# Optimization experiments

Measured on AMD Instinct MI355X. Metric: run time of the kernel, lower is better.

Reference implementation:

```python
import jax, jax.numpy as jnp
import numpy as np
import math

H = 300
B = 2048
SEG = 48
N = B * SEG

def _gru_direction(x_seq, h0, w_ih, w_hh, b_ih, b_hh, reverse):
    # x_seq: [L, B, H]; h0: [B, H]; w_ih/w_hh: [3H, H]; b_ih/b_hh: [3H]
    xp = jnp.einsum('lbh,gh->lbg', x_seq, w_ih) + b_ih  # precompute input projections [L,B,3H]
    def step(h, xp_t):
        hp = h @ w_hh.T + b_hh
        xr, xz, xn = jnp.split(xp_t, 3, axis=-1)
        hr, hz, hn = jnp.split(hp, 3, axis=-1)
        r = jax.nn.sigmoid(xr + hr)
        z = jax.nn.sigmoid(xz + hz)
        n = jnp.tanh(xn + r * hn)
        h_new = (1.0 - z) * n + z * h
        return h_new, h_new
    _, ys = jax.lax.scan(step, h0, xp, reverse=reverse)
    return ys  # [L, B, H]

def setup_inputs() -> dict:
    key = jax.random.key(0)
    ks = jax.random.split(key, 12)
    bound = 1.0 / math.sqrt(H)
    u = lambda k, shape: jax.random.uniform(k, shape, jnp.float32, -bound, bound)
    x = jax.random.normal(ks[0], (N, H), jnp.float32)
    batch = jnp.repeat(jnp.arange(B, dtype=jnp.int32), SEG)  # sorted segment ids
    return {
        'x': x,
        'batch': batch,
        'num_moles': B,
        'max_len': SEG,
        'bias': u(ks[1], (H,)),
        'w_ih_f': u(ks[2], (3 * H, H)),
        'w_hh_f': u(ks[3], (3 * H, H)),
        'b_ih_f': u(ks[4], (3 * H,)),
        'b_hh_f': u(ks[5], (3 * H,)),
        'w_ih_b': u(ks[6], (3 * H, H)),
        'w_hh_b': u(ks[7], (3 * H, H)),
        'b_ih_b': u(ks[8], (3 * H,)),
        'b_hh_b': u(ks[9], (3 * H,)),
    }

def reference(x, batch, num_moles, max_len, bias, w_ih_f, w_hh_f, b_ih_f, b_hh_f, w_ih_b, w_hh_b, b_ih_b, b_hh_b):
    n, h = x.shape
    message = jax.nn.relu(x + bias)
    counts = jax.ops.segment_sum(jnp.ones_like(batch), batch, num_segments=num_moles)
    offsets = jnp.cumsum(counts) - counts
    pos = jnp.arange(n, dtype=batch.dtype) - offsets[batch]  # position within molecule
    # ragged -> padded pack [B, L, H]
    padded = jnp.zeros((num_moles, max_len, h), x.dtype).at[batch, pos].set(message)
    # initial hidden = per-molecule max over raw x (same h0 for both directions)
    h0 = jax.ops.segment_max(x, batch, num_segments=num_moles)  # [B, H]
    xs = padded.transpose(1, 0, 2)  # [L, B, H]
    yf = _gru_direction(xs, h0, w_ih_f, w_hh_f, b_ih_f, b_hh_f, reverse=False)
    yb = _gru_direction(xs, h0, w_ih_b, w_hh_b, b_ih_b, b_hh_b, reverse=True)
    y = jnp.concatenate([yf, yb], axis=-1).transpose(1, 0, 2)  # [B, L, 2H]
    return y[batch, pos]  # unpad -> [N, 2H]
```

## Files before the change

### kernel.cpp

```cpp
#include <hip/hip_runtime.h>
#include <hip/hip_bf16.h>

#define H    300
#define KP   320
#define BM   2048
#define SEG  48
#define NTOK (BM*SEG)
#define G    900
#define GW   1024
#define XPW  912
#define MOLW 16
#define NCH  10
#define BKX  64

typedef __attribute__((ext_vector_type(8))) short short8;
typedef __attribute__((ext_vector_type(4))) float f32x4;

__device__ __forceinline__ float us2f(unsigned short u) { return __uint_as_float(((unsigned)u) << 16); }
__device__ __forceinline__ unsigned short bfb(float f) {
    __hip_bfloat16 b = __float2bfloat16(f);
    return *(unsigned short*)&b;
}
__device__ __forceinline__ void gload16(const void* g, void* l) {
    __builtin_amdgcn_global_load_lds((const __attribute__((address_space(1))) unsigned*)g,
                                     (__attribute__((address_space(3))) unsigned*)l, 16, 0, 0);
}

__global__ void prep_weights(const float* wih_f, const float* whh_f, const float* bih_f,
                             const float* wih_b, const float* whh_b, const float* bih_b,
                             __hip_bfloat16* wih, __hip_bfloat16* whh, float* bih) {
    int idx = blockIdx.x * 256 + threadIdx.x;
    const int wn = 2 * GW * KP;
    if (idx < wn) {
        int d = idx / (GW * KP);
        int R = (idx / KP) % GW;
        int k = idx % KP;
        int ct = R / 48, rem = R % 48, g = rem / 16, i = rem % 16;
        int col = ct * 16 + i;
        const float* src = d ? wih_b : wih_f;
        float v = (R < 912 && col < H && k < H) ? src[(g * H + col) * H + k] : 0.f;
        wih[idx] = __float2bfloat16(v);
        return;
    }
    idx -= wn;
    if (idx < wn) {
        int d = idx / (GW * KP);
        int R = (idx / KP) % GW;
        int k = idx % KP;
        int ct = R / 48, rem = R % 48, g = rem / 16, i = rem % 16;
        int col = ct * 16 + i;
        const float* src = d ? whh_b : whh_f;
        float v = (R < 912 && col < H && k < H) ? src[(g * H + col) * H + k] : 0.f;
        whh[idx] = __float2bfloat16(v);
        return;
    }
    idx -= wn;
    if (idx < 2 * GW) {
        int d = idx / GW;
        int R = idx % GW;
        int ct = R / 48, rem = R % 48, g = rem / 16, i = rem % 16;
        int col = ct * 16 + i;
        const float* src = d ? bih_b : bih_f;
        bih[idx] = (R < 912 && col < H) ? src[g * H + col] : 0.f;
    }
}

__global__ void prep_msg(const float* x, const float* bias, __hip_bfloat16* msg) {
    int idx = blockIdx.x * 256 + threadIdx.x;
    if (idx >= NTOK * KP) return;
    int i = idx / KP, k = idx % KP;
    float v = 0.f;
    if (k < H) {
        v = x[i * H + k] + bias[k];
        v = v > 0.f ? v : 0.f;
    }
    msg[idx] = __float2bfloat16(v);
}

__global__ void h0_kernel(const float* x, float* h0) {
    int m = blockIdx.x;
    for (int c = threadIdx.x; c < H; c += blockDim.x) {
        const float* base = x + (long long)m * SEG * H + c;
        float v = -INFINITY;
        for (int t = 0; t < SEG; t++) v = fmaxf(v, base[t * H]);
        h0[m * H + c] = v;
    }
}

__global__ __launch_bounds__(256) void xp_gemm(const __hip_bfloat16* msg, const __hip_bfloat16* wih,
                                               const float* bih, __hip_bfloat16* xp) {
    int d = blockIdx.z;
    const __hip_bfloat16* A  = msg;
    const __hip_bfloat16* Bw = wih + d * GW * KP;
    const float* bi = bih + d * GW;
    __hip_bfloat16* out = xp + (long long)d * NTOK * XPW;

    __shared__ __hip_bfloat16 sA[128 * BKX];
    __shared__ __hip_bfloat16 sB[128 * BKX];
    const short* sAs = (const short*)sA;
    const short* sBs = (const short*)sB;

    int tid = threadIdx.x;
    int lane = tid & 63, wid = tid >> 6;
    int l15 = lane & 15, quad = lane >> 4;
    int mblk = blockIdx.x * 128, nblk = blockIdx.y * 128;
    int mbase = (wid >> 1) * 64, nbase = (wid & 1) * 64;

    int srow = wid * 32 + (lane >> 3);
    int scc  = (lane & 7) ^ (srow & 7);
    const short* gA0 = (const short*)A  + (long long)(mblk + srow) * KP + scc * 8;
    const short* gB0 = (const short*)Bw + (long long)(nblk + srow) * KP + scc * 8;
    int xsw = (l15 & 7) << 3;

    f32x4 acc[4][4] = {};
    for (int kc = 0; kc < KP / BKX; kc++) {
#pragma unroll
        for (int j = 0; j < 4; j++)
            gload16(gA0 + (long long)j * 8 * KP + kc * BKX, (char*)sA + (wid * 4 + j) * 1024);
#pragma unroll
        for (int j = 0; j < 4; j++)
            gload16(gB0 + (long long)j * 8 * KP + kc * BKX, (char*)sB + (wid * 4 + j) * 1024);
        __syncthreads();

        short8 af[4][2], bf[4][2];
#pragma unroll
        for (int i = 0; i < 4; i++)
#pragma unroll
            for (int kh = 0; kh < 2; kh++)
                af[i][kh] = *(const short8*)(sAs + (mbase + i * 16 + l15) * BKX + ((kh * 32 + quad * 8) ^ xsw));
#pragma unroll
        for (int j = 0; j < 4; j++)
#pragma unroll
            for (int kh = 0; kh < 2; kh++)
                bf[j][kh] = *(const short8*)(sBs + (nbase + j * 16 + l15) * BKX + ((kh * 32 + quad * 8) ^ xsw));
#pragma unroll
        for (int i = 0; i < 4; i++)
#pragma unroll
            for (int j = 0; j < 4; j++) {
                acc[i][j] = __builtin_amdgcn_mfma_f32_16x16x32_bf16(af[i][0], bf[j][0], acc[i][j], 0, 0, 0);
                acc[i][j] = __builtin_amdgcn_mfma_f32_16x16x32_bf16(af[i][1], bf[j][1], acc[i][j], 0, 0, 0);
            }
        __syncthreads();
    }

#pragma unroll
    for (int i = 0; i < 4; i++)
#pragma unroll
        for (int j = 0; j < 4; j++) {
            int col = nblk + nbase + j * 16 + l15;
            if (col < XPW) {
                float bv = bi[col];
#pragma unroll
                for (int r = 0; r < 4; r++) {
                    int row = mblk + mbase + i * 16 + quad * 4 + r;
                    out[(long long)row * XPW + col] = __float2bfloat16(acc[i][j][r] + bv);
                }
            }
        }
}

__global__ __launch_bounds__(1024) void gru_kernel(const __hip_bfloat16* whh_all, const float* bhh_f,
                                                   const float* bhh_b, const __hip_bfloat16* xp,
                                                   const float* h0, float* out) {
    int grp = blockIdx.x;
    int d   = blockIdx.y;
    const char* whhd = (const char*)(whh_all + (long long)d * GW * KP);
    const float* bhh = d ? bhh_b : bhh_f;
    const __hip_bfloat16* xpd = xp + (long long)d * NTOK * XPW;

    int tid = threadIdx.x;
    int lane = tid & 63, wid = tid >> 6;
    int l15 = lane & 15, quad = lane >> 4;
    int xor3 = (l15 & 3) ^ ((l15 >> 2) & 3);

    __shared__ __hip_bfloat16 hB[MOLW * 328];
    __shared__ char bufA[65536];
    __shared__ char bufB[65536];

    int mol0 = grp * MOLW;

    const char* dmasrc[4];
#pragma unroll
    for (int j = 0; j < 4; j++) {
        int R = (wid * 4 + j) * 16 + (lane >> 2);
        int s = lane & 3;
        int sw = s ^ (R & 3) ^ ((R >> 2) & 3);
        dmasrc[j] = whhd + R * (KP * 2) + sw * 16;
    }

    int nct = (wid < 3) ? 2 : 1;

    for (int e = tid; e < MOLW * 328; e += 1024) hB[e] = __float2bfloat16(0.f);
    __syncthreads();

    float bvv[2][3];
    f32x4 hreg[2];
#pragma unroll
    for (int cc = 0; cc < 2; cc++) {
        if (cc < nct) {
            int ct = cc ? 16 + wid : wid;
            int col = ct * 16 + l15;
            bool cv = col < H;
#pragma unroll
            for (int g = 0; g < 3; g++)
                bvv[cc][g] = cv ? bhh[g * H + col] : 0.f;
#pragma unroll
            for (int r = 0; r < 4; r++) {
                float hv = cv ? h0[(size_t)(mol0 + quad * 4 + r) * H + col] : 0.f;
                hreg[cc][r] = hv;
                if (cv) hB[(quad * 4 + r) * 328 + col] = __float2bfloat16(hv);
            }
        }
    }

#pragma unroll
    for (int j = 0; j < 4; j++)
        gload16(dmasrc[j], bufA + (wid * 4 + j) * 1024);
    __syncthreads();

    for (int t = 0; t < SEG; t++) {
        int tt = d ? (SEG - 1 - t) : t;

        f32x4 acc[2][3] = {};
        unsigned short xv[2][3][4];

        auto phase = [&](int c, const char* curb, char* nxtb) {
            int nk = (c + 1) % NCH;
#pragma unroll
            for (int j = 0; j < 4; j++)
                gload16(dmasrc[j] + nk * 64, nxtb + (wid * 4 + j) * 1024);
            if (c == 8) {
#pragma unroll
                for (int cc = 0; cc < 2; cc++)
                    if (cc < nct) {
                        int ct = cc ? 16 + wid : wid;
#pragma unroll
                        for (int r = 0; r < 4; r++) {
                            long long tok = (long long)(mol0 + quad * 4 + r) * SEG + tt;
                            const unsigned short* xrow = (const unsigned short*)(xpd + tok * XPW + ct * 48 + l15);
#pragma unroll
                            for (int g = 0; g < 3; g++)
                                xv[cc][g][r] = xrow[g * 16];
                        }
                    }
            }
            short8 aq = *(const short8*)((const char*)hB + l15 * 656 + c * 64 + quad * 16);
#pragma unroll
            for (int cc = 0; cc < 2; cc++)
                if (cc < nct) {
                    int ct = cc ? 16 + wid : wid;
#pragma unroll
                    for (int g = 0; g < 3; g++) {
                        short8 bq = *(const short8*)(curb + (ct * 48 + g * 16 + l15) * 64 + ((quad ^ xor3) << 4));
                        acc[cc][g] = __builtin_amdgcn_mfma_f32_16x16x32_bf16(aq, bq, acc[cc][g], 0, 0, 0);
                    }
                }
            __syncthreads();
        };

#pragma unroll
        for (int c2 = 0; c2 < 5; c2++) {
            phase(2 * c2,     bufA, bufB);
            phase(2 * c2 + 1, bufB, bufA);
        }

#pragma unroll
        for (int cc = 0; cc < 2; cc++)
            if (cc < nct) {
                int ct = cc ? 16 + wid : wid;
                int col = ct * 16 + l15;
                bool cv = col < H;
#pragma unroll
                for (int r = 0; r < 4; r++) {
                    float hr = acc[cc][0][r] + bvv[cc][0];
                    float hz = acc[cc][1][r] + bvv[cc][1];
                    float hn = acc[cc][2][r] + bvv[cc][2];
                    float xr = us2f(xv[cc][0][r]);
                    float xz = us2f(xv[cc][1][r]);
                    float xn = us2f(xv[cc][2][r]);
                    float rg = 1.f / (1.f + __expf(-(xr + hr)));
                    float zg = 1.f / (1.f + __expf(-(xz + hz)));
                    float ni = xn + rg * hn;
                    float ng = 1.f - 2.f / (__expf(2.f * ni) + 1.f);
                    float hnew = (1.f - zg) * ng + zg * hreg[cc][r];
                    hreg[cc][r] = hnew;
                    if (cv) {
                        hB[(quad * 4 + r) * 328 + col] = __float2bfloat16(hnew);
                        long long tok = (long long)(mol0 + quad * 4 + r) * SEG + tt;
                        out[tok * 600 + d * 300 + col] = hnew;
                    }
                }
            }
        __syncthreads();
    }
}

extern "C" void kernel_launch(void* const* d_in, const int* in_sizes, int n_in,
                              void* d_out, int out_size, void* d_ws, size_t ws_size,
                              hipStream_t stream) {
    const float* x     = (const float*)d_in[0];
    const float* bias  = (const float*)d_in[4];
    const float* wih_f = (const float*)d_in[5];
    const float* whh_f = (const float*)d_in[6];
    const float* bih_f = (const float*)d_in[7];
    const float* bhh_f = (const float*)d_in[8];
    const float* wih_b = (const float*)d_in[9];
    const float* whh_b = (const float*)d_in[10];
    const float* bih_b = (const float*)d_in[11];
    const float* bhh_b = (const float*)d_in[12];
    float* out = (float*)d_out;

    char* ws = (char*)d_ws;
    __hip_bfloat16* msg = (__hip_bfloat16*)(ws);
    __hip_bfloat16* wih = (__hip_bfloat16*)(ws + 62914560LL);
    __hip_bfloat16* whh = (__hip_bfloat16*)(ws + 64225280LL);
    float*          bih = (float*)         (ws + 65536000LL);
    float*          h0  = (float*)         (ws + 65544192LL);
    __hip_bfloat16* xp  = (__hip_bfloat16*)(ws + 68001792LL);

    hipLaunchKernelGGL(prep_weights, dim3((2*GW*KP + 2*GW*KP + 2*GW + 255) / 256), dim3(256), 0, stream,
                       wih_f, whh_f, bih_f, wih_b, whh_b, bih_b, wih, whh, bih);
    hipLaunchKernelGGL(prep_msg, dim3((NTOK * KP + 255) / 256), dim3(256), 0, stream, x, bias, msg);
    hipLaunchKernelGGL(h0_kernel, dim3(BM), dim3(256), 0, stream, x, h0);
    hipLaunchKernelGGL(xp_gemm, dim3(NTOK / 128, GW / 128, 2), dim3(256), 0, stream, msg, wih, bih, xp);
    hipLaunchKernelGGL(gru_kernel, dim3(BM / MOLW, 2), dim3(1024), 0, stream, whh, bhh_f, bhh_b, xp, h0, out);
}
```

Before: 1.810 ms.

## Restructure GRU recurrence kernel: 32 molecules per block, staged gate epilogue

Each GRU block now processes 32 molecules instead of 16 using 512 threads. Every streamed W_hh chunk now feeds two MFMAs (two 16-row A tiles), which halves the weight traffic per molecule. The hidden projection is written as bf16 into the spent LDS buffer, and a separate element-pair pass computes the gates with vectorized xp/out accesses. It also uses explicit waitcnt/barrier pipelining and a block-index remap for the 128 blocks. In exchange, hp is rounded to bf16, each step gains an extra LDS round trip and barriers, and there are half as many blocks.

```diff
diff --git a/kernel.cpp b/kernel.cpp
--- a/kernel.cpp
+++ b/kernel.cpp
@@ -9,14 +9,18 @@
 #define G    900
 #define GW   1024
 #define XPW  912
-#define MOLW 16
+#define MOLW 32
+#define NPAIR (MOLW*150)
+#define PIT  10
+#define NT   57
 #define NCH  10
 #define BKX  64
 
 typedef __attribute__((ext_vector_type(8))) short short8;
 typedef __attribute__((ext_vector_type(4))) float f32x4;
 
-__device__ __forceinline__ float us2f(unsigned short u) { return __uint_as_float(((unsigned)u) << 16); }
+__device__ __forceinline__ float lo16(unsigned u) { return __uint_as_float(u << 16); }
+__device__ __forceinline__ float hi16(unsigned u) { return __uint_as_float(u & 0xffff0000u); }
 __device__ __forceinline__ unsigned short bfb(float f) {
     __hip_bfloat16 b = __float2bfloat16(f);
     return *(unsigned short*)&b;
@@ -25,6 +29,7 @@
     __builtin_amdgcn_global_load_lds((const __attribute__((address_space(1))) unsigned*)g,
                                      (__attribute__((address_space(3))) unsigned*)l, 16, 0, 0);
 }
+#define LBAR() do { asm volatile("s_waitcnt lgkmcnt(0)" ::: "memory"); __builtin_amdgcn_s_barrier(); } while (0)
 
 __global__ void prep_weights(const float* wih_f, const float* whh_f, const float* bih_f,
                              const float* wih_b, const float* whh_b, const float* bih_b,
@@ -159,11 +164,12 @@
         }
 }
 
-__global__ __launch_bounds__(1024) void gru_kernel(const __hip_bfloat16* whh_all, const float* bhh_f,
-                                                   const float* bhh_b, const __hip_bfloat16* xp,
-                                                   const float* h0, float* out) {
-    int grp = blockIdx.x;
-    int d   = blockIdx.y;
+__global__ __launch_bounds__(512, 2) void gru_kernel(const __hip_bfloat16* whh_all, const float* bhh_f,
+                                                     const float* bhh_b, const __hip_bfloat16* xp,
+                                                     const float* h0, float* out) {
+    int b = blockIdx.x;
+    int d = (b >> 2) & 1;
+    int grp = (b >> 3) * 4 + (b & 3);
     const char* whhd = (const char*)(whh_all + (long long)d * GW * KP);
     const float* bhh = d ? bhh_b : bhh_f;
     const __hip_bfloat16* xpd = xp + (long long)d * NTOK * XPW;
@@ -171,7 +177,6 @@
     int tid = threadIdx.x;
     int lane = tid & 63, wid = tid >> 6;
     int l15 = lane & 15, quad = lane >> 4;
-    int xor3 = (l15 & 3) ^ ((l15 >> 2) & 3);
 
     __shared__ __hip_bfloat16 hB[MOLW * 328];
     __shared__ char bufA[65536];
@@ -179,119 +184,150 @@
 
     int mol0 = grp * MOLW;
 
-    const char* dmasrc[4];
-#pragma unroll
-    for (int j = 0; j < 4; j++) {
-        int R = (wid * 4 + j) * 16 + (lane >> 2);
-        int s = lane & 3;
-        int sw = s ^ (R & 3) ^ ((R >> 2) & 3);
-        dmasrc[j] = whhd + R * (KP * 2) + sw * 16;
-    }
-
-    int nct = (wid < 3) ? 2 : 1;
-
-    for (int e = tid; e < MOLW * 328; e += 1024) hB[e] = __float2bfloat16(0.f);
+    const char* sb[8];
+#pragma unroll
+    for (int j = 0; j < 8; j++) {
+        int Gx = tid + j * 512;
+        int R = Gx >> 2;
+        int gsw = (Gx & 3) ^ (R & 3) ^ ((R >> 2) & 3);
+        sb[j] = whhd + R * (KP * 2) + gsw * 16;
+    }
+    int swz = (l15 & 3) ^ ((l15 >> 2) & 3);
+    int gq = ((quad ^ swz) & 3) << 4;
+
+    float bvw[8];
+#pragma unroll
+    for (int k = 0; k < 8; k++) {
+        int nt = wid + 8 * k;
+        float v = 0.f;
+        if (nt < NT) {
+            int gcol = nt * 16 + l15;
+            int ct = gcol / 48, rem = gcol % 48;
+            int g = rem >> 4, i = rem & 15;
+            int col = ct * 16 + i;
+            if (col < H) v = bhh[g * H + col];
+        }
+        bvw[k] = v;
+    }
+
+    for (int e = tid; e < MOLW * 328; e += 512) hB[e] = __float2bfloat16(0.f);
     __syncthreads();
 
-    float bvv[2][3];
-    f32x4 hreg[2];
-#pragma unroll
-    for (int cc = 0; cc < 2; cc++) {
-        if (cc < nct) {
-            int ct = cc ? 16 + wid : wid;
-            int col = ct * 16 + l15;
-            bool cv = col < H;
-#pragma unroll
-            for (int g = 0; g < 3; g++)
-                bvv[cc][g] = cv ? bhh[g * H + col] : 0.f;
-#pragma unroll
-            for (int r = 0; r < 4; r++) {
-                float hv = cv ? h0[(size_t)(mol0 + quad * 4 + r) * H + col] : 0.f;
-                hreg[cc][r] = hv;
-                if (cv) hB[(quad * 4 + r) * 328 + col] = __float2bfloat16(hv);
-            }
-        }
-    }
-
-#pragma unroll
-    for (int j = 0; j < 4; j++)
-        gload16(dmasrc[j], bufA + (wid * 4 + j) * 1024);
-    __syncthreads();
+    float hv0[PIT], hv1[PIT];
+#pragma unroll
+    for (int i = 0; i < PIT; i++) {
+        int e2 = tid + i * 512;
+        if (e2 < NPAIR) {
+            int m = e2 / 150, p = e2 % 150;
+            int c = (p >> 3) * 16 + (p & 7) * 2;
+            float2 hh = *(const float2*)(h0 + (size_t)(mol0 + m) * H + c);
+            hv0[i] = hh.x; hv1[i] = hh.y;
+            unsigned pack = ((unsigned)bfb(hh.y) << 16) | bfb(hh.x);
+            *(unsigned*)(&hB[m * 328 + c]) = pack;
+        }
+    }
+    LBAR();
+
+#pragma unroll
+    for (int j = 0; j < 8; j++)
+        gload16(sb[j], bufA + tid * 16 + j * 8192);
 
     for (int t = 0; t < SEG; t++) {
         int tt = d ? (SEG - 1 - t) : t;
-
-        f32x4 acc[2][3] = {};
-        unsigned short xv[2][3][4];
-
-        auto phase = [&](int c, const char* curb, char* nxtb) {
-            int nk = (c + 1) % NCH;
-#pragma unroll
-            for (int j = 0; j < 4; j++)
-                gload16(dmasrc[j] + nk * 64, nxtb + (wid * 4 + j) * 1024);
-            if (c == 8) {
-#pragma unroll
-                for (int cc = 0; cc < 2; cc++)
-                    if (cc < nct) {
-                        int ct = cc ? 16 + wid : wid;
-#pragma unroll
-                        for (int r = 0; r < 4; r++) {
-                            long long tok = (long long)(mol0 + quad * 4 + r) * SEG + tt;
-                            const unsigned short* xrow = (const unsigned short*)(xpd + tok * XPW + ct * 48 + l15);
-#pragma unroll
-                            for (int g = 0; g < 3; g++)
-                                xv[cc][g][r] = xrow[g * 16];
-                        }
+        char* be = (t & 1) ? bufB : bufA;
+        char* bo = (t & 1) ? bufA : bufB;
+
+        f32x4 acc[8][2] = {};
+#pragma unroll
+        for (int c = 0; c < NCH; c++) {
+            char* cur = (c & 1) ? bo : be;
+            char* nxt = (c & 1) ? be : bo;
+            if (c < NCH - 1) {
+#pragma unroll
+                for (int j = 0; j < 8; j++)
+                    gload16(sb[j] + (c + 1) * 64, nxt + tid * 16 + j * 8192);
+                asm volatile("s_waitcnt vmcnt(8)" ::: "memory");
+            } else {
+                asm volatile("s_waitcnt vmcnt(0)" ::: "memory");
+            }
+            __builtin_amdgcn_s_barrier();
+            short8 aq0 = *(const short8*)((const char*)hB + l15 * 656 + c * 64 + quad * 16);
+            short8 aq1 = *(const short8*)((const char*)hB + (16 + l15) * 656 + c * 64 + quad * 16);
+#pragma unroll
+            for (int k = 0; k < 8; k++) {
+                int nt = wid + 8 * k;
+                if (nt < NT) {
+                    short8 bq = *(const short8*)(cur + (nt * 16 + l15) * 64 + gq);
+                    acc[k][0] = __builtin_amdgcn_mfma_f32_16x16x32_bf16(aq0, bq, acc[k][0], 0, 0, 0);
+                    acc[k][1] = __builtin_amdgcn_mfma_f32_16x16x32_bf16(aq1, bq, acc[k][1], 0, 0, 0);
+                }
+            }
+            __builtin_amdgcn_s_barrier();
+        }
+
+#pragma unroll
+        for (int k = 0; k < 8; k++) {
+            int nt = wid + 8 * k;
+            if (nt < NT) {
+                int gcol = nt * 16 + l15;
+#pragma unroll
+                for (int rb = 0; rb < 2; rb++)
+#pragma unroll
+                    for (int r = 0; r < 4; r++) {
+                        int mol = rb * 16 + quad * 4 + r;
+                        *(__hip_bfloat16*)(be + mol * (XPW * 2) + gcol * 2) =
+                            __float2bfloat16(acc[k][rb][r] + bvw[k]);
                     }
             }
-            short8 aq = *(const short8*)((const char*)hB + l15 * 656 + c * 64 + quad * 16);
-#pragma unroll
-            for (int cc = 0; cc < 2; cc++)
-                if (cc < nct) {
-                    int ct = cc ? 16 + wid : wid;
-#pragma unroll
-                    for (int g = 0; g < 3; g++) {
-                        short8 bq = *(const short8*)(curb + (ct * 48 + g * 16 + l15) * 64 + ((quad ^ xor3) << 4));
-                        acc[cc][g] = __builtin_amdgcn_mfma_f32_16x16x32_bf16(aq, bq, acc[cc][g], 0, 0, 0);
-                    }
-                }
-            __syncthreads();
-        };
-
-#pragma unroll
-        for (int c2 = 0; c2 < 5; c2++) {
-            phase(2 * c2,     bufA, bufB);
-            phase(2 * c2 + 1, bufB, bufA);
-        }
-
-#pragma unroll
-        for (int cc = 0; cc < 2; cc++)
-            if (cc < nct) {
-                int ct = cc ? 16 + wid : wid;
-                int col = ct * 16 + l15;
-                bool cv = col < H;
-#pragma unroll
-                for (int r = 0; r < 4; r++) {
-                    float hr = acc[cc][0][r] + bvv[cc][0];
-                    float hz = acc[cc][1][r] + bvv[cc][1];
-                    float hn = acc[cc][2][r] + bvv[cc][2];
-                    float xr = us2f(xv[cc][0][r]);
-                    float xz = us2f(xv[cc][1][r]);
-                    float xn = us2f(xv[cc][2][r]);
-                    float rg = 1.f / (1.f + __expf(-(xr + hr)));
-                    float zg = 1.f / (1.f + __expf(-(xz + hz)));
-                    float ni = xn + rg * hn;
-                    float ng = 1.f - 2.f / (__expf(2.f * ni) + 1.f);
-                    float hnew = (1.f - zg) * ng + zg * hreg[cc][r];
-                    hreg[cc][r] = hnew;
-                    if (cv) {
-                        hB[(quad * 4 + r) * 328 + col] = __float2bfloat16(hnew);
-                        long long tok = (long long)(mol0 + quad * 4 + r) * SEG + tt;
-                        out[tok * 600 + d * 300 + col] = hnew;
-                    }
-                }
-            }
-        __syncthreads();
+        }
+        LBAR();
+
+#pragma unroll
+        for (int i = 0; i < PIT; i++) {
+            int e2 = tid + i * 512;
+            if (e2 < NPAIR) {
+                int m = e2 / 150, p = e2 % 150;
+                int ct = p >> 3, i2 = (p & 7) * 2;
+                int gib = ct * 48 + i2;
+                int c = ct * 16 + i2;
+                const __hip_bfloat16* hprow = (const __hip_bfloat16*)(be + m * (XPW * 2));
+                unsigned hr2 = *(const unsigned*)(hprow + gib);
+                unsigned hz2 = *(const unsigned*)(hprow + gib + 16);
+                unsigned hn2 = *(const unsigned*)(hprow + gib + 32);
+                long long tok = (long long)(mol0 + m) * SEG + tt;
+                const __hip_bfloat16* xrow = xpd + tok * XPW;
+                unsigned xr2 = *(const unsigned*)(xrow + gib);
+                unsigned xz2 = *(const unsigned*)(xrow + gib + 16);
+                unsigned xn2 = *(const unsigned*)(xrow + gib + 32);
+
+                float xr0 = lo16(xr2), xr1 = hi16(xr2);
+                float xz0 = lo16(xz2), xz1 = hi16(xz2);
+                float xn0 = lo16(xn2), xn1 = hi16(xn2);
+                float hr0 = lo16(hr2), hr1 = hi16(hr2);
+                float hz0 = lo16(hz2), hz1 = hi16(hz2);
+                float hn0 = lo16(hn2), hn1 = hi16(hn2);
+
+                float rg0 = 1.f / (1.f + __expf(-(xr0 + hr0)));
+                float rg1 = 1.f / (1.f + __expf(-(xr1 + hr1)));
+                float zg0 = 1.f / (1.f + __expf(-(xz0 + hz0)));
+                float zg1 = 1.f / (1.f + __expf(-(xz1 + hz1)));
+                float ni0 = xn0 + rg0 * hn0;
+                float ni1 = xn1 + rg1 * hn1;
+                float ng0 = 1.f - 2.f / (__expf(2.f * ni0) + 1.f);
+                float ng1 = 1.f - 2.f / (__expf(2.f * ni1) + 1.f);
+                float h0n = (1.f - zg0) * ng0 + zg0 * hv0[i];
+                float h1n = (1.f - zg1) * ng1 + zg1 * hv1[i];
+                hv0[i] = h0n; hv1[i] = h1n;
+
+                unsigned pack = ((unsigned)bfb(h1n) << 16) | bfb(h0n);
+                *(unsigned*)(&hB[m * 328 + c]) = pack;
+                *(float2*)(out + tok * 600 + d * 300 + c) = make_float2(h0n, h1n);
+            }
+        }
+#pragma unroll
+        for (int j = 0; j < 8; j++)
+            gload16(sb[j], bo + tid * 16 + j * 8192);
+        LBAR();
     }
 }
 
@@ -323,5 +359,5 @@
     hipLaunchKernelGGL(prep_msg, dim3((NTOK * KP + 255) / 256), dim3(256), 0, stream, x, bias, msg);
     hipLaunchKernelGGL(h0_kernel, dim3(BM), dim3(256), 0, stream, x, h0);
     hipLaunchKernelGGL(xp_gemm, dim3(NTOK / 128, GW / 128, 2), dim3(256), 0, stream, msg, wih, bih, xp);
-    hipLaunchKernelGGL(gru_kernel, dim3(BM / MOLW, 2), dim3(1024), 0, stream, whh, bhh_f, bhh_b, xp, h0, out);
-}
+    hipLaunchKernelGGL(gru_kernel, dim3(128), dim3(512), 0, stream, whh, bhh_f, bhh_b, xp, h0, out);
+}
```

New measurement: 2.431 ms. +34.3%, slower.
